# Kernel optimization log

Measured on AMD Instinct MI355X. Metric: run time of the kernel, lower is better.

The kernel has to match this reference:

```python
import jax, jax.numpy as jnp
import numpy as np
from jax import lax

B, C, H, W = 4, 256, 64, 64
C8 = C // 8


def _conv1x1(x, w, b):
    # x: (B,C,H,W), w: (O,C) -> (B,O,H,W)
    return jnp.einsum('bchw,oc->bohw', x, w) + b[None, :, None, None]


def setup_inputs() -> dict:
    key = jax.random.key(0)
    ks = jax.random.split(key, 9)
    s1 = 1.0 / np.sqrt(C)          # fan-in scale for 1x1 convs
    sf = 1.0 / np.sqrt(2 * C * 9)  # fan-in scale for 3x3 conv
    return {
        'front_x':     jax.random.normal(ks[0], (B, C, H, W), jnp.float32),
        'cross_x':     jax.random.normal(ks[1], (B, C, H, W), jnp.float32),
        'front_x_hat': jax.random.normal(ks[2], (B, C, H, W), jnp.float32),
        'Wq': jax.random.normal(ks[3], (C8, C), jnp.float32) * s1,
        'bq': jnp.zeros((C8,), jnp.float32),
        'Wk': jax.random.normal(ks[4], (C8, C), jnp.float32) * s1,
        'bk': jnp.zeros((C8,), jnp.float32),
        'Wv': jax.random.normal(ks[5], (C, C), jnp.float32) * s1,
        'bv': jnp.zeros((C,), jnp.float32),
        'Wf': jax.random.normal(ks[6], (C, 2 * C, 3, 3), jnp.float32) * sf,
        'bf': jnp.zeros((C,), jnp.float32),
    }


def reference(front_x, cross_x, front_x_hat, Wq, bq, Wk, bk, Wv, bv, Wf, bf):
    b, c, h, w = front_x.shape
    hw = h * w
    # projections -> (B, C/8, HW)
    q = _conv1x1(cross_x, Wq, bq).reshape(b, -1, hw)
    k = _conv1x1(front_x, Wk, bk).reshape(b, -1, hw)
    # energy[b,i,j] = <key_i, query_j>  (B, HW, HW)
    energy = jnp.einsum('bci,bcj->bij', k, q)
    front_star = jnp.max(energy, axis=1)     # (B, HW) best key score per query
    front_arg = jnp.argmax(energy, axis=1)   # (B, HW) best key index per query
    # value projection and hard gather of best-matching value per position
    v = _conv1x1(front_x_hat, Wv, bv).reshape(b, c, hw)
    T = jnp.take_along_axis(v, front_arg[:, None, :], axis=2).reshape(b, c, h, w)
    S = front_star.reshape(b, 1, h, w)
    cat = jnp.concatenate([front_x, T], axis=1)  # (B, 2C, H, W)
    res = lax.conv_general_dilated(
        cat, Wf, window_strides=(1, 1), padding='SAME',
        dimension_numbers=('NCHW', 'OIHW', 'NCHW')) + bf[None, :, None, None]
    return front_x + res * S
```

## Files before the change

### kernel.cpp

```cpp
#include <hip/hip_runtime.h>

#define Bn 4
#define Cn 256
#define C8 32
#define Hn 64
#define Wn 64
#define HWn 4096
#define PADR 80
#define ROWS (HWn + 2 * PADR)
#define MARGIN 6e-3f

typedef __bf16 bf16x8 __attribute__((ext_vector_type(8)));
typedef float floatx4 __attribute__((ext_vector_type(4)));
typedef unsigned short u16x8 __attribute__((ext_vector_type(8)));

__device__ __forceinline__ unsigned short f2bf(float f) {
  union { float f; unsigned int u; } c; c.f = f;
  unsigned int u = c.u;
  return (unsigned short)((u + 0x7FFFu + ((u >> 16) & 1u)) >> 16);
}
__device__ __forceinline__ float bf2f(unsigned short h) {
  union { unsigned int u; float f; } c; c.u = ((unsigned int)h) << 16;
  return c.f;
}
__device__ __forceinline__ void gl_lds16(const void* g, void* l) {
  __builtin_amdgcn_global_load_lds(
      (__attribute__((address_space(1))) void*)(uintptr_t)g,
      (__attribute__((address_space(3))) void*)(uintptr_t)l, 16, 0, 0);
}

__global__ __launch_bounds__(1024) void proj_cat_prep(
    const float* __restrict__ cross_x, const float* __restrict__ front_x,
    const float* __restrict__ front_hat,
    const float* __restrict__ Wq, const float* __restrict__ bq,
    const float* __restrict__ Wk, const float* __restrict__ bk,
    const float* __restrict__ Wv, const float* __restrict__ Wf,
    float* __restrict__ qf, float* __restrict__ kf,
    unsigned short* __restrict__ qhi, unsigned short* __restrict__ qlo,
    unsigned short* __restrict__ khi, unsigned short* __restrict__ klo,
    unsigned short* __restrict__ Wvb, unsigned short* __restrict__ Wfb,
    unsigned short* __restrict__ catF, unsigned short* __restrict__ xht,
    unsigned short* __restrict__ zpad, int* __restrict__ cnt) {
  union SMu {
    struct { float Wl[8192]; float part[3 * 4 * 8 * 64]; } pj;
    unsigned short tile[4][64][66];
  };
  __shared__ __align__(16) SMu sm;

  int bx = blockIdx.x;
  int tid1k = threadIdx.x;

  if (bx >= 1024) {
    size_t t = (size_t)(bx - 1024) * 1024 + tid1k;
    if (t == 0) cnt[0] = 0;
    if (t < 256) zpad[t] = 0;
    if (t < 131072) {
      const float* src = Wf + t * 9;
#pragma unroll
      for (int k = 0; k < 9; ++k)
        Wfb[(size_t)k * 131072 + t] = f2bf(src[k]);
    }
    if (t < 163840) {
      int col = (int)(t & 255);
      int r4 = (int)(t >> 8);
      int bb = r4 / 160, rr = r4 % 160;
      int row = (rr < PADR) ? rr : (HWn + rr);
      catF[((size_t)bb * ROWS + row) * 256 + col] = 0;
    }
    if (t < 65536) Wvb[t] = f2bf(Wv[t]);
    return;
  }

  if (bx >= 512) {
    int id = bx - 512;
    int j0 = (id & 63) * 64;
    int bz = id >> 6;
    int b = bz >> 1, which = bz & 1;
    int g4 = tid1k >> 8;
    int tid = tid1k & 255;
    int ci0 = g4 * 64;

    const float* src = (which == 0) ? front_x : front_hat;
#pragma unroll
    for (int u = tid; u < 1024; u += 256) {
      int cl = u >> 4, h4 = (u & 15) * 4;
      floatx4 v = *reinterpret_cast<const floatx4*>(
          &src[((size_t)(b * Cn + ci0 + cl)) * HWn + j0 + h4]);
#pragma unroll
      for (int k = 0; k < 4; ++k) sm.tile[g4][cl][h4 + k] = f2bf(v[k]);
    }
    __syncthreads();
#pragma unroll
    for (int u = tid; u < 512; u += 256) {
      int oct = u & 7, hw_l = u >> 3;
      u16x8 val;
#pragma unroll
      for (int k = 0; k < 8; ++k) val[k] = sm.tile[g4][oct * 8 + k][hw_l];
      if (which == 0)
        *reinterpret_cast<u16x8*>(
            &catF[((size_t)b * ROWS + PADR + j0 + hw_l) * 256 + ci0 + oct * 8]) = val;
      else
        *reinterpret_cast<u16x8*>(
            &xht[((size_t)b * HWn + j0 + hw_l) * 256 + ci0 + oct * 8]) = val;
    }
    return;
  }

  int id = bx;
  int tid = tid1k;
  int lane = tid & 63, wv = tid >> 6;
  int slice = wv & 3;
  int chunk = wv >> 2;
  int jb = id & 63;
  int b = (id >> 6) & 3;
  int z = id >> 8;
  int j = jb * 64 + lane;
  const float* x = (z == 0) ? cross_x : front_x;
  const float* Wraw = (z == 0) ? Wq : Wk;
  const float* bd = (z == 0) ? bq : bk;
  float* outp = (z == 0) ? qf : kf;
  unsigned short* hip_ = (z == 0) ? qhi : khi;
  unsigned short* lop_ = (z == 0) ? qlo : klo;
  int o0 = slice * 8;
  int c0 = chunk * 64;

  float* Wl = sm.pj.Wl;
  float* part = sm.pj.part;

  for (int u = tid; u < 8192; u += 1024) {
    int c = u >> 5, o = u & 31;
    Wl[u] = Wraw[o * 256 + c];
  }
  __syncthreads();

  const float* xb = x + (size_t)b * Cn * HWn + j;
  floatx4 a0 = (floatx4)0.0f, a1 = (floatx4)0.0f;
#pragma unroll 16
  for (int c = c0; c < c0 + 64; ++c) {
    float xv = xb[(size_t)c * HWn];
    floatx4 wa = *reinterpret_cast<const floatx4*>(&Wl[c * 32 + o0]);
    floatx4 wb = *reinterpret_cast<const floatx4*>(&Wl[c * 32 + o0 + 4]);
    a0 += wa * xv;
    a1 += wb * xv;
  }
  if (chunk > 0) {
    float* dst = &part[(((chunk - 1) * 4 + slice) * 8) * 64];
#pragma unroll
    for (int o = 0; o < 4; ++o) { dst[o * 64 + lane] = a0[o]; dst[(o + 4) * 64 + lane] = a1[o]; }
  }
  __syncthreads();
  if (chunk != 0) return;
#pragma unroll
  for (int q = 0; q < 3; ++q) {
    const float* src = &part[((q * 4 + slice) * 8) * 64];
#pragma unroll
    for (int o = 0; o < 4; ++o) { a0[o] += src[o * 64 + lane]; a1[o] += src[(o + 4) * 64 + lane]; }
  }
  float acc[8];
#pragma unroll
  for (int o = 0; o < 4; ++o) { acc[o] = a0[o] + bd[o0 + o]; acc[o + 4] = a1[o] + bd[o0 + 4 + o]; }

  float* op = outp + ((size_t)b * HWn + j) * C8 + o0;
  u16x8 hv, lv;
#pragma unroll
  for (int o = 0; o < 8; ++o) {
    op[o] = acc[o];
    unsigned short h = f2bf(acc[o]);
    hv[o] = h;
    lv[o] = f2bf(acc[o] - bf2f(h));
  }
  *reinterpret_cast<u16x8*>(hip_ + ((size_t)b * HWn + j) * C8 + o0) = hv;
  *reinterpret_cast<u16x8*>(lop_ + ((size_t)b * HWn + j) * C8 + o0) = lv;
}

__global__ __launch_bounds__(1024) void energy_approx(
    const unsigned short* __restrict__ khi, const unsigned short* __restrict__ klo,
    const unsigned short* __restrict__ qhi, const unsigned short* __restrict__ qlo,
    float* __restrict__ star, int* __restrict__ argb,
    int* __restrict__ cnt, int* __restrict__ list) {
  int b = blockIdx.y;
  int j0 = blockIdx.x * 32;
  int tid = threadIdx.x;
  int lane = tid & 63, wv = tid >> 6;
  int lm = lane & 15, lq = lane >> 4;

  __shared__ float bv1S[16][32];
  __shared__ int   bi1S[16][32];
  __shared__ float bv2S[16][32];

  bf16x8 qh[2], ql[2];
#pragma unroll
  for (int s = 0; s < 2; ++s) {
    int j = j0 + s * 16 + lm;
    qh[s] = *reinterpret_cast<const bf16x8*>(qhi + ((size_t)b * HWn + j) * 32 + lq * 8);
    ql[s] = *reinterpret_cast<const bf16x8*>(qlo + ((size_t)b * HWn + j) * 32 + lq * 8);
  }
  const unsigned short* kh_base = khi + (size_t)b * HWn * 32 + lq * 8;
  const unsigned short* kl_base = klo + (size_t)b * HWn * 32 + lq * 8;

  float b1[2], b2[2];
#pragma unroll
  for (int s = 0; s < 2; ++s) { b1[s] = -3.0e38f; b2[s] = -3.0e38f; }

  int ibase = wv * 256;
#pragma unroll 4
  for (int it = 0; it < 16; ++it) {
    int i0 = ibase + it * 16;
    bf16x8 ah = *reinterpret_cast<const bf16x8*>(kh_base + (size_t)(i0 + lm) * 32);
    bf16x8 al = *reinterpret_cast<const bf16x8*>(kl_base + (size_t)(i0 + lm) * 32);
#pragma unroll
    for (int s = 0; s < 2; ++s) {
      floatx4 acc = (floatx4)0.0f;
      acc = __builtin_amdgcn_mfma_f32_16x16x32_bf16(ah, qh[s], acc, 0, 0, 0);
      acc = __builtin_amdgcn_mfma_f32_16x16x32_bf16(ah, ql[s], acc, 0, 0, 0);
      acc = __builtin_amdgcn_mfma_f32_16x16x32_bf16(al, qh[s], acc, 0, 0, 0);
#pragma unroll
      for (int r = 0; r < 4; ++r) {
        unsigned code = (unsigned)(it * 4 + r);
        union { float f; unsigned u; } cv; cv.f = acc[r];
        cv.u = (cv.u & ~63u) | code;
        float vp = cv.f;
        b2[s] = __builtin_amdgcn_fmed3f(vp, b1[s], b2[s]);
        b1[s] = fmaxf(b1[s], vp);
      }
    }
  }
  int i1[2];
#pragma unroll
  for (int s = 0; s < 2; ++s) {
    union { float f; unsigned u; } cv; cv.f = b1[s];
    unsigned code = cv.u & 63u;
    i1[s] = ibase + (int)(code >> 2) * 16 + lq * 4 + (int)(code & 3u);
  }
#pragma unroll
  for (int s = 0; s < 2; ++s) {
#pragma unroll
    for (int m = 16; m <= 32; m <<= 1) {
      float ob1 = __shfl_xor(b1[s], m, 64);
      int oi1 = __shfl_xor(i1[s], m, 64);
      float ob2 = __shfl_xor(b2[s], m, 64);
      float c2;
      if (ob1 > b1[s] || (ob1 == b1[s] && oi1 < i1[s])) {
        c2 = fmaxf(b1[s], ob2);
        b1[s] = ob1; i1[s] = oi1;
      } else {
        c2 = fmaxf(ob1, b2[s]);
      }
      b2[s] = c2;
    }
    if (lq == 0) {
      bv1S[wv][s * 16 + lm] = b1[s];
      bi1S[wv][s * 16 + lm] = i1[s];
      bv2S[wv][s * 16 + lm] = b2[s];
    }
  }
  __syncthreads();
  if (tid < 32) {
    float B1 = bv1S[0][tid];
    int I1 = bi1S[0][tid];
    float B2 = bv2S[0][tid];
#pragma unroll
    for (int w = 1; w < 16; ++w) {
      float v1 = bv1S[w][tid];
      int ii = bi1S[w][tid];
      float v2 = bv2S[w][tid];
      if (v1 > B1) { B2 = fmaxf(B1, v2); B1 = v1; I1 = ii; }
      else B2 = fmaxf(B2, v1);
    }
    size_t o = (size_t)b * HWn + j0 + tid;
    union { float f; unsigned u; } cs; cs.f = B1;
    cs.u &= ~63u;
    star[o] = cs.f;
    argb[o] = I1;
    if (B1 - B2 < MARGIN) {
      int slot = atomicAdd(cnt, 1);
      list[slot] = (b << 12) | (j0 + (int)tid);
    }
  }
}

__global__ __launch_bounds__(256) void recheck_projv(
    const unsigned short* __restrict__ xht, const unsigned short* __restrict__ Wvb,
    const float* __restrict__ bv, unsigned short* __restrict__ vbf,
    const float* __restrict__ qf, const float* __restrict__ kf,
    const int* __restrict__ cnt, const int* __restrict__ list,
    float* __restrict__ star, int* __restrict__ argb) {
  int bx = blockIdx.x;
  if ((bx & 1) == 0) {
    int id = bx >> 1;
    int m0 = (id & 31) * 128;
    int o0 = ((id >> 5) & 1) * 128;
    int b = id >> 6;
    int tid = threadIdx.x;
    int lane = tid & 63, wv = tid >> 6;
    int wm = wv >> 1, wn = wv & 1;
    int lm = lane & 15, lq = lane >> 4;

    union SMu {
      struct { unsigned short A[2][128 * 32]; unsigned short B[2][128 * 32]; } st;
      unsigned short TS[128 * 136];
    };
    __shared__ __align__(16) SMu sm;

    floatx4 acc[4][4];
#pragma unroll
    for (int im = 0; im < 4; ++im)
#pragma unroll
      for (int in = 0; in < 4; ++in) acc[im][in] = (floatx4)0.0f;

    const int srow = lane >> 2;
    const int soff = (((lane & 3) ^ ((lane >> 3) & 3)) * 8);
    const int sa = (lq ^ ((lm >> 1) & 3)) * 8;
    const unsigned short* ag = Wvb + (size_t)o0 * 256;
    const unsigned short* bg = xht + ((size_t)b * HWn + m0) * 256;

    auto STAGE = [&](int buf, int kc) {
#pragma unroll
      for (int i = 0; i < 2; ++i) {
        int r0 = wv * 32 + i * 16;
        gl_lds16(ag + ((size_t)(r0 + srow)) * 256 + kc + soff, &sm.st.A[buf][r0 * 32]);
        gl_lds16(bg + ((size_t)(r0 + srow)) * 256 + kc + soff, &sm.st.B[buf][r0 * 32]);
      }
    };
    auto COMPUTE = [&](int buf) {
      bf16x8 afr[4];
#pragma unroll
      for (int im = 0; im < 4; ++im)
        afr[im] = *reinterpret_cast<const bf16x8*>(
            &sm.st.A[buf][(wm * 64 + im * 16 + lm) * 32 + sa]);
#pragma unroll
      for (int in = 0; in < 4; ++in) {
        bf16x8 bfr = *reinterpret_cast<const bf16x8*>(
            &sm.st.B[buf][(wn * 64 + in * 16 + lm) * 32 + sa]);
#pragma unroll
        for (int im = 0; im < 4; ++im)
          acc[im][in] = __builtin_amdgcn_mfma_f32_16x16x32_bf16(
              afr[im], bfr, acc[im][in], 0, 0, 0);
      }
    };

    STAGE(0, 0);
#pragma unroll 2
    for (int st = 0; st < 8; ++st) {
      __builtin_amdgcn_s_barrier();
      if (st < 7) {
        STAGE((st + 1) & 1, (st + 1) * 32);
        asm volatile("s_waitcnt vmcnt(4)" ::: "memory");
      } else {
        asm volatile("s_waitcnt vmcnt(0)" ::: "memory");
      }
      __builtin_amdgcn_s_barrier();
      __builtin_amdgcn_sched_barrier(0);
      COMPUTE(st & 1);
    }
    __builtin_amdgcn_s_barrier();

#pragma unroll
    for (int in = 0; in < 4; ++in) {
      int pl = wn * 64 + in * 16 + lm;
#pragma unroll
      for (int im = 0; im < 4; ++im) {
#pragma unroll
        for (int r = 0; r < 4; ++r) {
          int ol = wm * 64 + im * 16 + lq * 4 + r;
          sm.TS[pl * 136 + ol] = f2bf(acc[im][in][r] + bv[o0 + ol]);
        }
      }
    }
    __syncthreads();
    for (int idx = tid; idx < 128 * 16; idx += 256) {
      int p = idx >> 4, ch = idx & 15;
      u16x8 val = *reinterpret_cast<const u16x8*>(&sm.TS[p * 136 + ch * 8]);
      *reinterpret_cast<u16x8*>(
          &vbf[((size_t)b * HWn + m0 + p) * 256 + o0 + ch * 8]) = val;
    }
  } else {
    __shared__ double bvS[4];
    __shared__ int biS[4];
    int n = cnt[0];
    int tid = threadIdx.x;
    int lane = tid & 63, wv = tid >> 6;
    for (int idx = bx >> 1; idx < n; idx += 256) {
      int e = list[idx];
      int b = e >> 12, j = e & 4095;
      const float* qp = qf + ((size_t)b * HWn + j) * 32;
      double qj[32];
#pragma unroll
      for (int o = 0; o < 32; ++o) qj[o] = (double)qp[o];
      double best = -1.0e300;
      int bi = 1 << 30;
      for (int i = tid; i < HWn; i += 256) {
        const float* kp = kf + ((size_t)b * HWn + i) * 32;
        double s = 0.0;
#pragma unroll
        for (int o = 0; o < 32; ++o) s += (double)kp[o] * qj[o];
        if (s > best) { best = s; bi = i; }
      }
#pragma unroll
      for (int m = 1; m < 64; m <<= 1) {
        double ob = __shfl_xor(best, m, 64);
        int oi = __shfl_xor(bi, m, 64);
        if (ob > best || (ob == best && oi < bi)) { best = ob; bi = oi; }
      }
      if (lane == 0) { bvS[wv] = best; biS[wv] = bi; }
      __syncthreads();
      if (tid == 0) {
#pragma unroll
        for (int w = 1; w < 4; ++w) {
          if (bvS[w] > best || (bvS[w] == best && biS[w] < bi)) {
            best = bvS[w]; bi = biS[w];
          }
        }
        star[(size_t)b * HWn + j] = (float)best;
        argb[(size_t)b * HWn + j] = bi;
      }
      __syncthreads();
    }
  }
}

__global__ __launch_bounds__(256) void conv_mfma(
    const unsigned short* __restrict__ catF, const unsigned short* __restrict__ Wfb,
    const unsigned short* __restrict__ vbf, const int* __restrict__ argb,
    const unsigned short* __restrict__ zpad, unsigned short* __restrict__ Pg) {
  int m0 = blockIdx.x * 128;
  int o0 = blockIdx.y * 128;
  int bz = blockIdx.z;
  int b = bz / 3, g = bz % 3;
  int dy = g - 1;
  int tid = threadIdx.x;
  int lane = tid & 63;
  int wv = tid >> 6;
  int wm = wv >> 1, wn = wv & 1;
  int lm = lane & 15, lq = lane >> 4;
  const bool lane_first = (lm == 0);
  const bool lane_last = (lm == 15);

  __shared__ __align__(16) unsigned short AS[2][3 * 128 * 32];
  __shared__ __align__(16) unsigned short BS[2][144 * 32];

  floatx4 acc[4][4];
#pragma unroll
  for (int im = 0; im < 4; ++im)
#pragma unroll
    for (int in = 0; in < 4; ++in) acc[im][in] = (floatx4)0.0f;

  const int srow = lane >> 2;
  const int soff = (((lane & 3) ^ ((lane >> 3) & 3)) * 8);
  const int sa = (lq ^ ((lm >> 1) & 3)) * 8;
  const unsigned short* catb =
      catF + ((size_t)b * ROWS + PADR + m0 + dy * 64 - 1) * 256;
  const unsigned short* ag = Wfb + ((size_t)(g * 3) * 256 + o0) * 512;

  auto mk_tsrc = [&](int s) -> const unsigned short* {
    int p = m0 + dy * 64 - 1 + s * 16 + srow;
    bool v = ((unsigned)p < (unsigned)HWn);
    int aj = argb[(size_t)b * HWn + (v ? p : 0)];
    return v ? (vbf + ((size_t)b * HWn + aj) * 256) : zpad;
  };
  const unsigned short* tP0 = mk_tsrc(wv);
  const unsigned short* tP1 = mk_tsrc(wv + 4);
  const unsigned short* tP2 = (wv == 0) ? mk_tsrc(8) : zpad;
  const int s0 = wv, s1 = wv + 4;

  auto STAGE = [&](unsigned short* ASb, unsigned short* BSb, int kc) {
#pragma unroll
    for (int i = 0; i < 6; ++i) {
      int l = wv + i * 4;
      int t = l >> 3, s = l & 7;
      gl_lds16(ag + ((size_t)(t * 256 + s * 16 + srow)) * 512 + kc + soff,
               &ASb[(t * 128 + s * 16) * 32]);
    }
    if (kc < 256) {
      gl_lds16(catb + ((size_t)(s0 * 16 + srow)) * 256 + kc + soff,
               &BSb[(s0 * 16) * 32]);
      gl_lds16(catb + ((size_t)(s1 * 16 + srow)) * 256 + kc + soff,
               &BSb[(s1 * 16) * 32]);
      if (wv == 0)
        gl_lds16(catb + ((size_t)(8 * 16 + srow)) * 256 + kc + soff,
                 &BSb[(8 * 16) * 32]);
    } else {
      int kk = kc - 256;
      gl_lds16(tP0 + kk + soff, &BSb[(s0 * 16) * 32]);
      gl_lds16(tP1 + kk + soff, &BSb[(s1 * 16) * 32]);
      if (wv == 0)
        gl_lds16(tP2 + kk + soff, &BSb[(8 * 16) * 32]);
    }
  };
  auto COMPUTE = [&](const unsigned short* ASb, const unsigned short* BSb) {
#pragma unroll
    for (int t = 0; t < 3; ++t) {
      bf16x8 afr[4];
#pragma unroll
      for (int im = 0; im < 4; ++im)
        afr[im] = *reinterpret_cast<const bf16x8*>(
            &ASb[(t * 128 + wm * 64 + im * 16 + lm) * 32 + sa]);
#pragma unroll
      for (int in = 0; in < 4; ++in) {
        int u = wn * 64 + in * 16 + lm + t;
        int sb = (lq ^ ((u >> 1) & 3)) * 8;
        u16x8 braw = *reinterpret_cast<const u16x8*>(&BSb[u * 32 + sb]);
        if ((t == 0 && in == 0 && lane_first) ||
            (t == 2 && in == 3 && lane_last))
          braw = (u16x8)(unsigned short)0;
        union { u16x8 u8; bf16x8 h; } cvt; cvt.u8 = braw;
#pragma unroll
        for (int im = 0; im < 4; ++im)
          acc[im][in] = __builtin_amdgcn_mfma_f32_16x16x32_bf16(
              afr[im], cvt.h, acc[im][in], 0, 0, 0);
      }
    }
  };

  STAGE(AS[0], BS[0], 0);
  __syncthreads();
  for (int kci = 0; kci < 16; kci += 2) {
    if (kci < 15) STAGE(AS[1], BS[1], (kci + 1) * 32);
    COMPUTE(AS[0], BS[0]);
    __syncthreads();
    if (kci < 14) STAGE(AS[0], BS[0], (kci + 2) * 32);
    COMPUTE(AS[1], BS[1]);
    __syncthreads();
  }

  unsigned short* P = Pg + ((size_t)(g * Bn + b) * Cn) * HWn;
#pragma unroll
  for (int in = 0; in < 4; ++in) {
    int p = m0 + wn * 64 + in * 16 + lm;
#pragma unroll
    for (int im = 0; im < 4; ++im) {
      int ob = o0 + wm * 64 + im * 16 + lq * 4;
#pragma unroll
      for (int r = 0; r < 4; ++r)
        P[(size_t)(ob + r) * HWn + p] = f2bf(acc[im][in][r]);
    }
  }
}

__global__ __launch_bounds__(256) void combine(
    const unsigned short* __restrict__ Pg, const float* __restrict__ fx,
    const float* __restrict__ bf, const float* __restrict__ star,
    float* __restrict__ out) {
  size_t e = ((size_t)blockIdx.x * 256 + threadIdx.x) * 8;
  int p = (int)(e & 4095);
  int bo = (int)(e >> 12);
  int o = bo & 255, b = bo >> 8;
  const size_t gs = (size_t)Bn * Cn * HWn;
  u16x8 q0 = *reinterpret_cast<const u16x8*>(Pg + e);
  u16x8 q1 = *reinterpret_cast<const u16x8*>(Pg + gs + e);
  u16x8 q2 = *reinterpret_cast<const u16x8*>(Pg + 2 * gs + e);
  float bias = bf[o];
  const float* sp = star + (size_t)b * HWn + p;
  const float* fp = fx + e;
  float* op = out + e;
#pragma unroll
  for (int h = 0; h < 2; ++h) {
    floatx4 s = *reinterpret_cast<const floatx4*>(sp + h * 4);
    floatx4 f = *reinterpret_cast<const floatx4*>(fp + h * 4);
    floatx4 r;
#pragma unroll
    for (int i = 0; i < 4; ++i) {
      int k = h * 4 + i;
      float a = bf2f(q0[k]) + bf2f(q1[k]) + bf2f(q2[k]);
      r[i] = f[i] + (a + bias) * s[i];
    }
    *reinterpret_cast<floatx4*>(op + h * 4) = r;
  }
}

extern "C" void kernel_launch(void* const* d_in, const int* in_sizes, int n_in,
                              void* d_out, int out_size, void* d_ws, size_t ws_size,
                              hipStream_t stream) {
  const float* front_x   = (const float*)d_in[0];
  const float* cross_x   = (const float*)d_in[1];
  const float* front_hat = (const float*)d_in[2];
  const float* Wq = (const float*)d_in[3];
  const float* bq = (const float*)d_in[4];
  const float* Wk = (const float*)d_in[5];
  const float* bk = (const float*)d_in[6];
  const float* Wv = (const float*)d_in[7];
  const float* bv = (const float*)d_in[8];
  const float* Wf = (const float*)d_in[9];
  const float* bf = (const float*)d_in[10];
  float* out = (float*)d_out;

  char* ws = (char*)d_ws;
  size_t off = 0;
  auto alloc = [&](size_t bytes) -> void* {
    void* p = (void*)(ws + off);
    off += (bytes + 255) & ~(size_t)255;
    return p;
  };
  unsigned short* Wvb = (unsigned short*)alloc(65536 * sizeof(unsigned short));
  unsigned short* Wfb = (unsigned short*)alloc((size_t)9 * 256 * 512 * sizeof(unsigned short));
  float* qf  = (float*)alloc((size_t)Bn * HWn * C8 * sizeof(float));
  float* kf  = (float*)alloc((size_t)Bn * HWn * C8 * sizeof(float));
  unsigned short* qhi = (unsigned short*)alloc((size_t)Bn * HWn * C8 * 2);
  unsigned short* qlo = (unsigned short*)alloc((size_t)Bn * HWn * C8 * 2);
  unsigned short* khi = (unsigned short*)alloc((size_t)Bn * HWn * C8 * 2);
  unsigned short* klo = (unsigned short*)alloc((size_t)Bn * HWn * C8 * 2);
  float*  star = (float*)alloc((size_t)Bn * HWn * sizeof(float));
  int*    argb = (int*)alloc((size_t)Bn * HWn * sizeof(int));
  int*    cnt  = (int*)alloc(256);
  int*    list = (int*)alloc((size_t)Bn * HWn * sizeof(int));
  unsigned short* xht = (unsigned short*)alloc((size_t)Bn * HWn * 256 * 2);
  unsigned short* vbf = (unsigned short*)alloc((size_t)Bn * HWn * 256 * 2);
  unsigned short* catF = (unsigned short*)alloc((size_t)Bn * ROWS * 256 * sizeof(unsigned short));
  unsigned short* zpad = (unsigned short*)alloc(256 * sizeof(unsigned short));
  unsigned short* Pg = (unsigned short*)alloc((size_t)3 * Bn * Cn * HWn * 2);

  proj_cat_prep<<<dim3(1184), dim3(1024), 0, stream>>>(
      cross_x, front_x, front_hat, Wq, bq, Wk, bk, Wv, Wf,
      qf, kf, qhi, qlo, khi, klo, Wvb, Wfb, catF, xht, zpad, cnt);

  energy_approx<<<dim3(HWn / 32, Bn), dim3(1024), 0, stream>>>(
      khi, klo, qhi, qlo, star, argb, cnt, list);

  recheck_projv<<<dim3(512), dim3(256), 0, stream>>>(
      xht, Wvb, bv, vbf, qf, kf, cnt, list, star, argb);

  conv_mfma<<<dim3(HWn / 128, Cn / 128, Bn * 3), dim3(256), 0, stream>>>(
      catF, Wfb, vbf, argb, zpad, Pg);

  combine<<<dim3((Bn * Cn * HWn / 8) / 256), dim3(256), 0, stream>>>(
      Pg, front_x, bf, star, out);
}
```

Measured before the change: 222.2 us.

## Fuse combine into conv kernel via last-arriving-block atomic tickets

```diff
diff --git a/kernel.cpp b/kernel.cpp
--- a/kernel.cpp
+++ b/kernel.cpp
@@ -40,7 +40,8 @@
     unsigned short* __restrict__ khi, unsigned short* __restrict__ klo,
     unsigned short* __restrict__ Wvb, unsigned short* __restrict__ Wfb,
     unsigned short* __restrict__ catF, unsigned short* __restrict__ xht,
-    unsigned short* __restrict__ zpad, int* __restrict__ cnt) {
+    unsigned short* __restrict__ zpad, int* __restrict__ cnt,
+    int* __restrict__ tickets) {
   union SMu {
     struct { float Wl[8192]; float part[3 * 4 * 8 * 64]; } pj;
     unsigned short tile[4][64][66];
@@ -53,7 +54,7 @@
   if (bx >= 1024) {
     size_t t = (size_t)(bx - 1024) * 1024 + tid1k;
     if (t == 0) cnt[0] = 0;
-    if (t < 256) zpad[t] = 0;
+    if (t < 256) { zpad[t] = 0; tickets[t] = 0; }
     if (t < 131072) {
       const float* src = Wf + t * 9;
 #pragma unroll
@@ -422,7 +423,10 @@
 __global__ __launch_bounds__(256) void conv_mfma(
     const unsigned short* __restrict__ catF, const unsigned short* __restrict__ Wfb,
     const unsigned short* __restrict__ vbf, const int* __restrict__ argb,
-    const unsigned short* __restrict__ zpad, unsigned short* __restrict__ Pg) {
+    const unsigned short* __restrict__ zpad, unsigned short* __restrict__ Pg,
+    const float* __restrict__ fx, const float* __restrict__ bfc,
+    const float* __restrict__ star, float* __restrict__ out,
+    int* __restrict__ tickets) {
   int m0 = blockIdx.x * 128;
   int o0 = blockIdx.y * 128;
   int bz = blockIdx.z;
@@ -438,6 +442,7 @@
 
   __shared__ __align__(16) unsigned short AS[2][3 * 128 * 32];
   __shared__ __align__(16) unsigned short BS[2][144 * 32];
+  __shared__ int lastS;
 
   floatx4 acc[4][4];
 #pragma unroll
@@ -535,36 +540,44 @@
         P[(size_t)(ob + r) * HWn + p] = f2bf(acc[im][in][r]);
     }
   }
-}
-
-__global__ __launch_bounds__(256) void combine(
-    const unsigned short* __restrict__ Pg, const float* __restrict__ fx,
-    const float* __restrict__ bf, const float* __restrict__ star,
-    float* __restrict__ out) {
-  size_t e = ((size_t)blockIdx.x * 256 + threadIdx.x) * 8;
-  int p = (int)(e & 4095);
-  int bo = (int)(e >> 12);
-  int o = bo & 255, b = bo >> 8;
+
+  __threadfence();
+  __syncthreads();
+  if (tid == 0) {
+    int tIdx = ((b * (HWn / 128) + (int)blockIdx.x) * (Cn / 128) + (int)blockIdx.y);
+    lastS = atomicAdd(&tickets[tIdx], 1);
+  }
+  __syncthreads();
+  if (lastS != 2) return;
+  __threadfence();
+
   const size_t gs = (size_t)Bn * Cn * HWn;
-  u16x8 q0 = *reinterpret_cast<const u16x8*>(Pg + e);
-  u16x8 q1 = *reinterpret_cast<const u16x8*>(Pg + gs + e);
-  u16x8 q2 = *reinterpret_cast<const u16x8*>(Pg + 2 * gs + e);
-  float bias = bf[o];
-  const float* sp = star + (size_t)b * HWn + p;
-  const float* fp = fx + e;
-  float* op = out + e;
-#pragma unroll
-  for (int h = 0; h < 2; ++h) {
-    floatx4 s = *reinterpret_cast<const floatx4*>(sp + h * 4);
-    floatx4 f = *reinterpret_cast<const floatx4*>(fp + h * 4);
-    floatx4 r;
-#pragma unroll
-    for (int i = 0; i < 4; ++i) {
-      int k = h * 4 + i;
-      float a = bf2f(q0[k]) + bf2f(q1[k]) + bf2f(q2[k]);
-      r[i] = f[i] + (a + bias) * s[i];
-    }
-    *reinterpret_cast<floatx4*>(op + h * 4) = r;
+  for (int u = tid; u < 2048; u += 256) {
+    int o_l = u >> 4;
+    int p8 = (u & 15) * 8;
+    int o_abs = o0 + o_l;
+    int p = m0 + p8;
+    size_t e = ((size_t)(b * Cn + o_abs)) * HWn + p;
+    u16x8 q0 = *reinterpret_cast<const u16x8*>(Pg + e);
+    u16x8 q1 = *reinterpret_cast<const u16x8*>(Pg + gs + e);
+    u16x8 q2 = *reinterpret_cast<const u16x8*>(Pg + 2 * gs + e);
+    float bias = bfc[o_abs];
+    const float* sp = star + (size_t)b * HWn + p;
+    const float* fp = fx + e;
+    float* op = out + e;
+#pragma unroll
+    for (int h = 0; h < 2; ++h) {
+      floatx4 s = *reinterpret_cast<const floatx4*>(sp + h * 4);
+      floatx4 f = *reinterpret_cast<const floatx4*>(fp + h * 4);
+      floatx4 r;
+#pragma unroll
+      for (int i = 0; i < 4; ++i) {
+        int k = h * 4 + i;
+        float a = bf2f(q0[k]) + bf2f(q1[k]) + bf2f(q2[k]);
+        r[i] = f[i] + (a + bias) * s[i];
+      }
+      *reinterpret_cast<floatx4*>(op + h * 4) = r;
+    }
   }
 }
 
@@ -607,11 +620,12 @@
   unsigned short* vbf = (unsigned short*)alloc((size_t)Bn * HWn * 256 * 2);
   unsigned short* catF = (unsigned short*)alloc((size_t)Bn * ROWS * 256 * sizeof(unsigned short));
   unsigned short* zpad = (unsigned short*)alloc(256 * sizeof(unsigned short));
+  int* tickets = (int*)alloc(256 * sizeof(int));
   unsigned short* Pg = (unsigned short*)alloc((size_t)3 * Bn * Cn * HWn * 2);
 
   proj_cat_prep<<<dim3(1184), dim3(1024), 0, stream>>>(
       cross_x, front_x, front_hat, Wq, bq, Wk, bk, Wv, Wf,
-      qf, kf, qhi, qlo, khi, klo, Wvb, Wfb, catF, xht, zpad, cnt);
+      qf, kf, qhi, qlo, khi, klo, Wvb, Wfb, catF, xht, zpad, cnt, tickets);
 
   energy_approx<<<dim3(HWn / 32, Bn), dim3(1024), 0, stream>>>(
       khi, klo, qhi, qlo, star, argb, cnt, list);
@@ -620,8 +634,5 @@
       xht, Wvb, bv, vbf, qf, kf, cnt, list, star, argb);
 
   conv_mfma<<<dim3(HWn / 128, Cn / 128, Bn * 3), dim3(256), 0, stream>>>(
-      catF, Wfb, vbf, argb, zpad, Pg);
-
-  combine<<<dim3((Bn * Cn * HWn / 8) / 256), dim3(256), 0, stream>>>(
-      Pg, front_x, bf, star, out);
-}
+      catF, Wfb, vbf, argb, zpad, Pg, front_x, bf, star, out, tickets);
+}
```

After: 374.2 us. 1.68x slower.
